# Kernel optimization log

Hardware: AMD Instinct MI355X
Metric: run time of the kernel (lower is better)

## Reference

```python
import jax, jax.numpy as jnp
import numpy as np

N_GENES = 8192      # input genes
WM = 4              # width_multiplier: hidden nodes per gene
HID = N_GENES * WM  # 32768 hidden units
N_TF = 1024         # embedding dim (TF activities)
GPT = 64            # target genes per TF in the prior network
BATCH = 256
EPS = 1e-5          # BatchNorm1d eps


def _connectivity():
    # layer1: hidden node h belongs to gene h // WM (fan_in = 1)
    rows1 = np.arange(HID, dtype=np.int32)
    cols1 = (rows1 // WM).astype(np.int32)
    # layer2: fully connected within each gene group (WM x WM blocks)
    rows2 = np.repeat(np.arange(HID, dtype=np.int32), WM)
    cols2 = (((np.arange(HID)[:, None] // WM) * WM) + np.arange(WM)).astype(np.int32).ravel()
    # layer3: each TF connects to all WM nodes of GPT randomly chosen genes
    rng = np.random.default_rng(0)
    genes = rng.integers(0, N_GENES, size=(N_TF, GPT))
    cols3 = (genes[:, :, None] * WM + np.arange(WM)).astype(np.int32).reshape(-1)
    rows3 = np.repeat(np.arange(N_TF, dtype=np.int32), GPT * WM)
    return rows1, cols1, rows2, cols2, rows3, cols3


def _sparse_linear(x, w, b, rows, cols, out_dim):
    # y[b, o] = sum_{e: rows[e]==o} w[e] * x[b, cols[e]] + b[o]
    xe = x[:, cols] * w  # [B, E]
    y = jnp.zeros((x.shape[0], out_dim), x.dtype).at[:, rows].add(xe)
    return y + b


def _batchnorm(x):
    # BatchNorm1d(affine=False), training mode: biased batch var
    m = jnp.mean(x, axis=0)
    v = jnp.var(x, axis=0)
    return (x - m) / jnp.sqrt(v + EPS)


def setup_inputs() -> dict:
    key = jax.random.key(0)
    k = jax.random.split(key, 7)
    rows1, cols1, rows2, cols2, rows3, cols3 = _connectivity()
    inp = {
        "features": jax.random.normal(k[0], (BATCH, N_GENES), jnp.float32),
        "w1": jax.random.normal(k[1], (HID,), jnp.float32),                 # fan_in 1
        "b1": jax.random.normal(k[2], (HID,), jnp.float32) * 0.01,
        "w2": jax.random.normal(k[3], (HID * WM,), jnp.float32) / np.sqrt(WM),
        "b2": jax.random.normal(k[4], (HID,), jnp.float32) * 0.01,
        "w3": jax.random.normal(k[5], (N_TF * GPT * WM,), jnp.float32) / np.sqrt(GPT * WM),
        "b3": jax.random.normal(k[6], (N_TF,), jnp.float32) * 0.01,
        "rows1": jnp.asarray(rows1), "cols1": jnp.asarray(cols1),
        "rows2": jnp.asarray(rows2), "cols2": jnp.asarray(cols2),
        "rows3": jnp.asarray(rows3), "cols3": jnp.asarray(cols3),
    }
    return inp


def reference(features, w1, b1, w2, b2, w3, b3,
              rows1, cols1, rows2, cols2, rows3, cols3):
    h = _sparse_linear(features, w1, b1, rows1, cols1, HID)
    h = _batchnorm(jax.nn.relu(h))
    h = _sparse_linear(h, w2, b2, rows2, cols2, HID)
    h = _batchnorm(jax.nn.relu(h))
    z = _sparse_linear(h, w3, b3, rows3, cols3, N_TF)
    return _batchnorm(z)
```

## Files before the change

### kernel.cpp

```cpp
#include <hip/hip_runtime.h>
#include <cstddef>

#define EPS 1e-5f

constexpr int NG  = 8192;
constexpr int HID = 32768;
constexpr int NTF = 1024;
constexpr int B   = 256;

static __device__ __forceinline__ unsigned short f2bf(float v) {
    union { float f; unsigned u; } a; a.f = v;
    unsigned r = a.u + 0x7fffu + ((a.u >> 16) & 1u);
    return (unsigned short)(r >> 16);
}

__global__ __launch_bounds__(256) void fused12(
    const float* __restrict__ x,
    const float* __restrict__ w1,
    const float* __restrict__ b1,
    const float* __restrict__ w2,
    const float* __restrict__ b2,
    unsigned short* __restrict__ h2rT,
    float* __restrict__ inv2g)
{
    const int lane  = threadIdx.x & 63;
    const int slice = threadIdx.x >> 6;
    const int c     = (blockIdx.x << 6) + lane;
    const int g     = c >> 2;
    const int b0    = slice << 6;

    __shared__ float redA[4][64], redB[4][64];
    __shared__ float m1s[64], inv1s[64];

    const float w1c = w1[c], b1c = b1[c];
    const float* xp = x + (size_t)b0 * NG + g;

    float s = 0.f, s2 = 0.f;
    #pragma unroll 8
    for (int i = 0; i < 64; ++i) {
        float h = fmaxf(fmaf(w1c, xp[(size_t)i * NG], b1c), 0.f);
        s += h;
        s2 = fmaf(h, h, s2);
    }
    redA[slice][lane] = s;
    redB[slice][lane] = s2;
    __syncthreads();
    if (slice == 0) {
        float S  = redA[0][lane] + redA[1][lane] + redA[2][lane] + redA[3][lane];
        float S2 = redB[0][lane] + redB[1][lane] + redB[2][lane] + redB[3][lane];
        float m  = S * (1.f / 256.f);
        float v  = fmaf(-m, m, S2 * (1.f / 256.f));
        m1s[lane]   = m;
        inv1s[lane] = rsqrtf(v + EPS);
    }
    __syncthreads();

    const int lbase = lane & ~3;
    const int gbase = g << 2;
    float w1j[4], b1j[4], w2s[4];
    float bconst = b2[c];
    #pragma unroll
    for (int j = 0; j < 4; ++j) {
        w1j[j] = w1[gbase + j];
        b1j[j] = b1[gbase + j];
        float wv = w2[(c << 2) + j] * inv1s[lbase + j];
        w2s[j] = wv;
        bconst = fmaf(-wv, m1s[lbase + j], bconst);
    }

    float t2s = 0.f, t2s2 = 0.f;
    unsigned short* op = h2rT + (size_t)c * B + b0;
    for (int i0 = 0; i0 < 64; i0 += 4) {
        ushort4 pk;
        unsigned short* pp = (unsigned short*)&pk;
        #pragma unroll
        for (int u = 0; u < 4; ++u) {
            float v = xp[(size_t)(i0 + u) * NG];
            float acc = bconst;
            #pragma unroll
            for (int j = 0; j < 4; ++j) {
                float r = fmaxf(fmaf(w1j[j], v, b1j[j]), 0.f);
                acc = fmaf(w2s[j], r, acc);
            }
            float r2 = fmaxf(acc, 0.f);
            t2s += r2;
            t2s2 = fmaf(r2, r2, t2s2);
            pp[u] = f2bf(r2);
        }
        *(ushort4*)(op + i0) = pk;
    }

    __syncthreads();
    redA[slice][lane] = t2s;
    redB[slice][lane] = t2s2;
    __syncthreads();
    if (slice == 0) {
        float S  = redA[0][lane] + redA[1][lane] + redA[2][lane] + redA[3][lane];
        float S2 = redB[0][lane] + redB[1][lane] + redB[2][lane] + redB[3][lane];
        float m  = S * (1.f / 256.f);
        float v  = fmaf(-m, m, S2 * (1.f / 256.f));
        inv2g[c] = rsqrtf(v + EPS);
    }
}

__global__ __launch_bounds__(256) void prep3(
    const float* __restrict__ w3,
    const int*   __restrict__ cols3,
    const float* __restrict__ inv2g,
    float* __restrict__ wfold,
    int*   __restrict__ colb)
{
    const int i = (blockIdx.x << 8) + threadIdx.x;
    const int col = cols3[i];
    wfold[i] = w3[i] * inv2g[col];
    colb[i]  = col << 9;
}

__global__ __launch_bounds__(256) void gather3(
    const unsigned short* __restrict__ h2,
    const float* __restrict__ wfold,
    const int*   __restrict__ colb,
    float* __restrict__ zraw)
{
    const int slice = blockIdx.x & 7;
    const int t     = blockIdx.x >> 3;
    const int tid   = threadIdx.x;

    __shared__ float wls[256];
    __shared__ int   alds[256];
    __shared__ float sred[16][33];

    wls[tid]  = wfold[(t << 8) + tid];
    alds[tid] = colb[(t << 8) + tid];
    __syncthreads();

    const int eg = tid >> 4;
    const int r2 = tid & 15;
    const int boff = (slice << 6) + (r2 << 2);
    const char* h2c = (const char*)h2;

    float a0 = 0.f, a1 = 0.f;
    #pragma unroll
    for (int k = 0; k < 16; ++k) {
        const int e = (k << 4) | eg;
        float w = wls[e];
        unsigned u = *(const unsigned*)(h2c + alds[e] + boff);
        union { unsigned v; float f; } lo, hi;
        lo.v = u << 16;
        hi.v = u & 0xffff0000u;
        a0 = fmaf(w, lo.f, a0);
        a1 = fmaf(w, hi.f, a1);
    }
    sred[eg][(r2 << 1)]     = a0;
    sred[eg][(r2 << 1) + 1] = a1;
    __syncthreads();

    if (tid < 32) {
        float s = 0.f;
        #pragma unroll
        for (int e = 0; e < 16; ++e) s += sred[e][tid];
        zraw[(t << 8) + (slice << 5) + tid] = s;
    }
}

__global__ __launch_bounds__(256) void bn3(
    const float* __restrict__ zraw,
    float* __restrict__ out)
{
    const int t   = blockIdx.x;
    const int tid = threadIdx.x;
    __shared__ float rs[4], rs2[4];

    float z = zraw[(t << 8) + tid];
    float s = z, s2 = z * z;
    #pragma unroll
    for (int o = 32; o > 0; o >>= 1) {
        s  += __shfl_xor(s, o);
        s2 += __shfl_xor(s2, o);
    }
    if ((tid & 63) == 0) { rs[tid >> 6] = s; rs2[tid >> 6] = s2; }
    __syncthreads();
    float S  = rs[0] + rs[1] + rs[2] + rs[3];
    float S2 = rs2[0] + rs2[1] + rs2[2] + rs2[3];
    float m  = S * (1.f / 256.f);
    float v  = fmaf(-m, m, S2 * (1.f / 256.f));
    out[(size_t)tid * NTF + t] = (z - m) * rsqrtf(v + EPS);
}

extern "C" void kernel_launch(void* const* d_in, const int* in_sizes, int n_in,
                              void* d_out, int out_size, void* d_ws, size_t ws_size,
                              hipStream_t stream) {
    const float* x   = (const float*)d_in[0];
    const float* w1  = (const float*)d_in[1];
    const float* b1  = (const float*)d_in[2];
    const float* w2  = (const float*)d_in[3];
    const float* b2  = (const float*)d_in[4];
    const float* w3  = (const float*)d_in[5];
    const float* b3  = (const float*)d_in[6];  (void)b3;
    const int* cols3 = (const int*)d_in[12];
    float* out = (float*)d_out;

    unsigned short* h2rT = (unsigned short*)d_ws;
    float* inv2g = (float*)(h2rT + (size_t)HID * B);
    float* wfold = inv2g + HID;
    int*   colb  = (int*)(wfold + NTF * 256);
    float* zraw  = (float*)(colb + NTF * 256);

    fused12<<<HID / 64, 256, 0, stream>>>(x, w1, b1, w2, b2, h2rT, inv2g);
    prep3  <<<NTF,      256, 0, stream>>>(w3, cols3, inv2g, wfold, colb);
    gather3<<<NTF * 8,  256, 0, stream>>>(h2rT, wfold, colb, zraw);
    bn3    <<<NTF,      256, 0, stream>>>(zraw, out);
}
```

Before: 121.9 us.

## Stage h2 writes through LDS and use async global-to-LDS loads in gather3

In fused12, the bf16 h2 outputs are first gathered into a shared-memory tile, so each wave writes whole 512-byte rows to global memory instead of scattered 8-byte stores. In gather3, each block now takes half a batch row range for one TF. It pulls the 256 gathered rows straight into LDS with global_load_lds and then accumulates from LDS, using 2 blocks per TF instead of 8. The trade-off is a large LDS footprint (64 KB tile), which limits occupancy, plus one LDS round trip. The per-row async loads are also only 4 bytes per lane.

```diff
diff --git a/kernel.cpp b/kernel.cpp
--- a/kernel.cpp
+++ b/kernel.cpp
@@ -7,6 +7,10 @@
 constexpr int HID = 32768;
 constexpr int NTF = 1024;
 constexpr int B   = 256;
+
+typedef __attribute__((address_space(3))) void  lds_void;
+typedef __attribute__((address_space(1))) const void g_void;
+#define GLDS(gp, lp) __builtin_amdgcn_global_load_lds((g_void*)(gp), (lds_void*)(lp), 4, 0, 0)
 
 static __device__ __forceinline__ unsigned short f2bf(float v) {
     union { float f; unsigned u; } a; a.f = v;
@@ -31,6 +35,7 @@
 
     __shared__ float redA[4][64], redB[4][64];
     __shared__ float m1s[64], inv1s[64];
+    __shared__ unsigned short tile[64][260];
 
     const float w1c = w1[c], b1c = b1[c];
     const float* xp = x + (size_t)b0 * NG + g;
@@ -69,7 +74,6 @@
     }
 
     float t2s = 0.f, t2s2 = 0.f;
-    unsigned short* op = h2rT + (size_t)c * B + b0;
     for (int i0 = 0; i0 < 64; i0 += 4) {
         ushort4 pk;
         unsigned short* pp = (unsigned short*)&pk;
@@ -87,12 +91,24 @@
             t2s2 = fmaf(r2, r2, t2s2);
             pp[u] = f2bf(r2);
         }
-        *(ushort4*)(op + i0) = pk;
+        *(ushort4*)&tile[lane][b0 + i0] = pk;
     }
 
     __syncthreads();
     redA[slice][lane] = t2s;
     redB[slice][lane] = t2s2;
+
+    {
+        const int w = slice;
+        char* hb = (char*)h2rT;
+        #pragma unroll 4
+        for (int cc = 0; cc < 16; ++cc) {
+            const int cl = (w << 4) + cc;
+            ushort4 v = *(const ushort4*)&tile[cl][lane << 2];
+            *(ushort4*)(hb + (((size_t)(blockIdx.x << 6) + cl) << 9) + (lane << 3)) = v;
+        }
+    }
+
     __syncthreads();
     if (slice == 0) {
         float S  = redA[0][lane] + redA[1][lane] + redA[2][lane] + redA[3][lane];
@@ -122,45 +138,41 @@
     const int*   __restrict__ colb,
     float* __restrict__ zraw)
 {
-    const int slice = blockIdx.x & 7;
-    const int t     = blockIdx.x >> 3;
-    const int tid   = threadIdx.x;
-
+    const int t    = blockIdx.x >> 1;
+    const int half = blockIdx.x & 1;
+    const int tid  = threadIdx.x;
+
+    __shared__ unsigned short tile[256][128];
     __shared__ float wls[256];
-    __shared__ int   alds[256];
-    __shared__ float sred[16][33];
-
-    wls[tid]  = wfold[(t << 8) + tid];
-    alds[tid] = colb[(t << 8) + tid];
-    __syncthreads();
-
-    const int eg = tid >> 4;
-    const int r2 = tid & 15;
-    const int boff = (slice << 6) + (r2 << 2);
-    const char* h2c = (const char*)h2;
-
-    float a0 = 0.f, a1 = 0.f;
-    #pragma unroll
-    for (int k = 0; k < 16; ++k) {
-        const int e = (k << 4) | eg;
-        float w = wls[e];
-        unsigned u = *(const unsigned*)(h2c + alds[e] + boff);
-        union { unsigned v; float f; } lo, hi;
-        lo.v = u << 16;
-        hi.v = u & 0xffff0000u;
-        a0 = fmaf(w, lo.f, a0);
-        a1 = fmaf(w, hi.f, a1);
-    }
-    sred[eg][(r2 << 1)]     = a0;
-    sred[eg][(r2 << 1) + 1] = a1;
-    __syncthreads();
-
-    if (tid < 32) {
-        float s = 0.f;
-        #pragma unroll
-        for (int e = 0; e < 16; ++e) s += sred[e][tid];
-        zraw[(t << 8) + (slice << 5) + tid] = s;
-    }
+    __shared__ float sred[2][128];
+
+    const int cb = colb[(t << 8) + tid] + (half << 8);
+    wls[tid] = wfold[(t << 8) + tid];
+
+    const int w    = tid >> 6;
+    const int lane = tid & 63;
+    const char* hb = (const char*)h2;
+    for (int j = 0; j < 64; ++j) {
+        const int e  = (w << 6) + j;
+        const int cbe = __shfl(cb, j, 64);
+        GLDS(hb + cbe + (lane << 2), &tile[e][0]);
+    }
+    __syncthreads();
+
+    const int eh = tid >> 7;
+    const int r  = tid & 127;
+    float acc = 0.f;
+    #pragma unroll 8
+    for (int e = 0; e < 128; ++e) {
+        const int ee = (eh << 7) + e;
+        union { unsigned u; float f; } cv;
+        cv.u = (unsigned)tile[ee][r] << 16;
+        acc = fmaf(wls[ee], cv.f, acc);
+    }
+    sred[eh][r] = acc;
+    __syncthreads();
+    if (tid < 128)
+        zraw[(t << 8) + (half << 7) + tid] = sred[0][tid] + sred[1][tid];
 }
 
 __global__ __launch_bounds__(256) void bn3(
@@ -208,6 +220,6 @@
 
     fused12<<<HID / 64, 256, 0, stream>>>(x, w1, b1, w2, b2, h2rT, inv2g);
     prep3  <<<NTF,      256, 0, stream>>>(w3, cols3, inv2g, wfold, colb);
-    gather3<<<NTF * 8,  256, 0, stream>>>(h2rT, wfold, colb, zraw);
+    gather3<<<NTF * 2,  256, 0, stream>>>(h2rT, wfold, colb, zraw);
     bn3    <<<NTF,      256, 0, stream>>>(zraw, out);
 }
```

Result: no change. 123.1 us (+1.0%).
